# Kernel optimization log

Hardware: AMD Instinct MI355X
Metric: run time of the kernel (lower is better)

Reference implementation:

```python
import jax, jax.numpy as jnp
import numpy as np

N_NODES = 100000
N_EDGES = 3200000
NFEAT, H1, H2, NCLASS = 512, 300, 200, 40


def setup_inputs() -> dict:
    key = jax.random.key(0)
    ks = jax.random.split(key, 8)
    x = jax.random.normal(ks[0], (N_NODES, NFEAT), dtype=jnp.float32)
    edge_index = jax.random.randint(ks[1], (2, N_EDGES), 0, N_NODES, dtype=jnp.int32)
    edge_weight = jax.random.uniform(ks[2], (N_EDGES,), dtype=jnp.float32)
    def glorot(k, fi, fo):
        s = 1.0 / np.sqrt(fi)
        return jax.random.uniform(k, (fi, fo), jnp.float32, -s, s)
    w1 = glorot(ks[3], NFEAT, H1)
    w2 = glorot(ks[4], H1, H2)
    w3 = glorot(ks[5], H2, NCLASS)
    return {
        'x': x, 'edge_index': edge_index, 'edge_weight': edge_weight,
        'w1': w1, 'b1': jnp.zeros((H1,), jnp.float32),
        'w2': w2, 'b2': jnp.zeros((H2,), jnp.float32),
        'w3': w3, 'b3': jnp.zeros((NCLASS,), jnp.float32),
    }


def _gcn_layer(h, edge_index, edge_weight, w, b):
    # support = h @ W ; out = A @ support + b  (A given as weighted edge list)
    support = h @ w                                   # [N, out]
    src, dst = edge_index[0], edge_index[1]
    msgs = support[src] * edge_weight[:, None]        # gather + scale, [E, out]
    agg = jax.ops.segment_sum(msgs, dst, num_segments=h.shape[0])
    return agg + b


def reference(x, edge_index, edge_weight, w1, b1, w2, b2, w3, b3):
    h1 = jax.nn.relu(_gcn_layer(x, edge_index, edge_weight, w1, b1))
    h2 = jax.nn.relu(_gcn_layer(h1, edge_index, edge_weight, w2, b2))
    logits = _gcn_layer(h2, edge_index, edge_weight, w3, b3)
    return jax.nn.softmax(logits, axis=1)
```

## Files before the change

kernel.cpp:

```cpp
#include <hip/hip_runtime.h>
#include <hip/hip_bf16.h>
#include <hip/hip_fp16.h>
#include <math.h>

#define NFEAT 512
#define H1 300
#define H2 200
#define NCLASS 40

typedef __attribute__((ext_vector_type(8))) _Float16 half8;
typedef __attribute__((ext_vector_type(4))) float f32x4;
typedef __attribute__((ext_vector_type(2))) unsigned int u32x2;

__device__ __forceinline__ void stage16(const void* gptr, void* ldsptr) {
    __builtin_amdgcn_global_load_lds(
        (const __attribute__((address_space(1))) unsigned int*)gptr,
        (__attribute__((address_space(3))) unsigned int*)ldsptr,
        16, 0, 0);
}

__device__ __forceinline__ unsigned short f2h(float f) {
    return __half_as_ushort(__float2half(f));
}
__device__ __forceinline__ float h2f(unsigned short u) {
    return __half2float(__ushort_as_half(u));
}
__device__ __forceinline__ float2 h2f2(unsigned int u) {
    __half2 h = *reinterpret_cast<__half2*>(&u);
    return __half22float2(h);
}
__device__ __forceinline__ unsigned pack2h(float a, float b) {
    return (unsigned)f2h(a) | ((unsigned)f2h(b) << 16);
}


__global__ __launch_bounds__(256) void count_dst_kernel(const int* __restrict__ dst,
                                                        int* __restrict__ counts, int E) {
    int i = blockIdx.x * blockDim.x + threadIdx.x;
    if (i < E) atomicAdd(&counts[dst[i]], 1);
}

__global__ __launch_bounds__(1024) void scan_kernel(const int* __restrict__ counts,
                                                    int* __restrict__ row_ptr,
                                                    int* __restrict__ nextp, int N) {
    __shared__ int sums[1024];
    const int tid = threadIdx.x;
    const int CH = (N + 1023) >> 10;
    const int b = tid * CH;
    const int e = min(b + CH, N);
    int s = 0;
    for (int i = b; i < e; i++) s += counts[i];
    sums[tid] = s;
    __syncthreads();
    #pragma unroll
    for (int off = 1; off < 1024; off <<= 1) {
        int t = (tid >= off) ? sums[tid - off] : 0;
        __syncthreads();
        sums[tid] += t;
        __syncthreads();
    }
    int run = (tid > 0) ? sums[tid - 1] : 0;
    for (int i = b; i < e; i++) {
        row_ptr[i] = run;
        nextp[i] = run;
        run += counts[i];
    }
    if (tid == 0) row_ptr[N] = sums[1023];
}

__global__ __launch_bounds__(256) void fill_csr_kernel(const int* __restrict__ src,
                                                       const int* __restrict__ dst,
                                                       const float* __restrict__ ew,
                                                       int* __restrict__ next,
                                                       int2* __restrict__ csr_sw, int E) {
    int i = blockIdx.x * blockDim.x + threadIdx.x;
    if (i < E) {
        int d = dst[i];
        int pos = atomicAdd(&next[d], 1);
        csr_sw[pos] = make_int2(src[i], __float_as_int(ew[i]));
    }
}


__global__ __launch_bounds__(256) void cvt_x_kernel(const float* __restrict__ in,
                                                    unsigned short* __restrict__ out,
                                                    size_t n4) {
    size_t i = (size_t)blockIdx.x * 256 + threadIdx.x;
    if (i < n4) {
        float4 a = ((const float4*)in)[i];
        u32x2 w;
        w.x = pack2h(a.x, a.y);
        w.y = pack2h(a.z, a.w);
        *(u32x2*)(out + i * 4) = w;
    }
}


__global__ __launch_bounds__(256) void split_weights_kernel(
        const float* __restrict__ w1, const float* __restrict__ w2, const float* __restrict__ w3,
        unsigned short* __restrict__ W1H, unsigned short* __restrict__ W1L,
        unsigned short* __restrict__ W2H, unsigned short* __restrict__ W2L,
        unsigned short* __restrict__ W3H, unsigned short* __restrict__ W3L) {
    int i = blockIdx.x * 256 + threadIdx.x;
    const float* w; unsigned short *H, *L; int K, N, KP;
    if (i < 163840) {
        w = w1; H = W1H; L = W1L; K = 512; N = 300; KP = 512;
    } else if (i < 163840 + 81920) {
        i -= 163840; w = w2; H = W2H; L = W2L; K = 300; N = 200; KP = 320;
    } else {
        i -= 245760; w = w3; H = W3H; L = W3L; K = 200; N = 40; KP = 256;
    }
    int n = i / KP, k = i - n * KP;
    float a = (n < N && k < K) ? w[(size_t)k * N + n] : 0.f;
    unsigned short h = f2h(a);
    H[i] = h;
    L[i] = f2h(a - h2f(h));
}


template <int KPAD, int NT>
__global__ __launch_bounds__(256, 3) void gemm_f16_kernel(
        const unsigned short* __restrict__ A,
        const unsigned short* __restrict__ Bhi, const unsigned short* __restrict__ Blo,
        unsigned short* __restrict__ C, int M, int NP, int MT) {
    extern __shared__ short lds[];
    short* As    = lds;
    short* Bs_hi = lds + 16384;
    short* Bs_lo = lds + 20480;

    const int id = blockIdx.x;
    const int g  = id / (8 * NT);
    const int r  = id % (8 * NT);
    const int nt = r >> 3;
    const int x  = r & 7;
    const int mt = g * 8 + x;
    if (mt >= MT) return;

    const int tid = threadIdx.x;
    const int wave = tid >> 6, lane = tid & 63;
    const int lm = lane & 15, quad = lane >> 4;
    const int bm = mt * 256, bn = nt * 64;

    f32x4 acc[4][4] = {};

    for (int k0 = 0; k0 < KPAD; k0 += 64) {
        #pragma unroll
        for (int i = 0; i < 8; i++) {
            int t = i * 256 + tid;
            int m = t >> 3;
            int c = (t & 7) ^ (m & 7);
            int row = bm + m; row = row < M ? row : M - 1;
            size_t goff = (size_t)row * KPAD + (size_t)(k0 + c * 8);
            int lbase = (i * 256 + wave * 64) * 8;
            stage16(A + goff, As + lbase);
        }
        #pragma unroll
        for (int i = 0; i < 2; i++) {
            int t = i * 256 + tid;
            int n = t >> 3;
            int c = (t & 7) ^ (n & 7);
            size_t goff = (size_t)(bn + n) * KPAD + (size_t)(k0 + c * 8);
            int lbase = (i * 256 + wave * 64) * 8;
            stage16(Bhi + goff, Bs_hi + lbase);
            stage16(Blo + goff, Bs_lo + lbase);
        }
        __syncthreads();

        #pragma unroll
        for (int h = 0; h < 2; h++) {
            const int cidx = h * 4 + quad;
            half8 a[4], bh[4], bl[4];
            #pragma unroll
            for (int i = 0; i < 4; i++) {
                int m = wave * 64 + i * 16 + lm;
                int off = (m * 8 + (cidx ^ (m & 7))) * 8;
                a[i] = *(const half8*)(As + off);
            }
            #pragma unroll
            for (int j = 0; j < 4; j++) {
                int n = j * 16 + lm;
                int off = (n * 8 + (cidx ^ (n & 7))) * 8;
                bh[j] = *(const half8*)(Bs_hi + off);
                bl[j] = *(const half8*)(Bs_lo + off);
            }
            #pragma unroll
            for (int i = 0; i < 4; i++)
                #pragma unroll
                for (int j = 0; j < 4; j++) {
                    acc[i][j] = __builtin_amdgcn_mfma_f32_16x16x32_f16(a[i], bh[j], acc[i][j], 0, 0, 0);
                    acc[i][j] = __builtin_amdgcn_mfma_f32_16x16x32_f16(a[i], bl[j], acc[i][j], 0, 0, 0);
                }
        }
        __syncthreads();
    }

    #pragma unroll
    for (int i = 0; i < 4; i++) {
        #pragma unroll
        for (int j = 0; j < 4; j++) {
            #pragma unroll
            for (int r2 = 0; r2 < 4; r2++) {
                int row = bm + wave * 64 + i * 16 + quad * 4 + r2;
                int col = bn + j * 16 + lm;
                if (row < M)
                    C[(size_t)row * NP + col] = f2h(acc[i][j][r2]);
            }
        }
    }
}


template <int F, int NP>
__global__ __launch_bounds__(256) void spmm_relu_f16_kernel(
        const int* __restrict__ row_ptr, const int2* __restrict__ csr_sw,
        const unsigned short* __restrict__ support, const float* __restrict__ bias,
        unsigned short* __restrict__ outp, int N) {
    constexpr int F4 = F / 4;
    constexpr int NP4 = NP / 4;
    constexpr int NCH = (F4 + 63) / 64;
    constexpr int NCHW = (NP4 + 63) / 64;

    int row = blockIdx.x * 4 + (threadIdx.x >> 6);
    int lane = threadIdx.x & 63;
    if (row >= N) return;
    int beg = row_ptr[row], end = row_ptr[row + 1];

    float acc[NCHW][4] = {};

    int e = beg;
    for (; e + 3 < end; e += 4) {
        int s_[4]; float w_[4];
        #pragma unroll
        for (int q = 0; q < 4; q++) {
            int2 sw = csr_sw[e + q];
            s_[q] = __builtin_amdgcn_readfirstlane(sw.x);
            w_[q] = __uint_as_float((unsigned)__builtin_amdgcn_readfirstlane(sw.y));
        }
        u32x2 u[4][NCH];
        #pragma unroll
        for (int q = 0; q < 4; q++) {
            const unsigned short* sp = support + (size_t)s_[q] * NP;
            #pragma unroll
            for (int j = 0; j < NCH; j++) {
                int f4 = j * 64 + lane;
                if (f4 < F4) u[q][j] = *(const u32x2*)(sp + f4 * 4);
            }
        }
        #pragma unroll
        for (int q = 0; q < 4; q++) {
            #pragma unroll
            for (int j = 0; j < NCH; j++) {
                int f4 = j * 64 + lane;
                if (f4 < F4) {
                    float2 a0 = h2f2(u[q][j].x), a1 = h2f2(u[q][j].y);
                    acc[j][0] += w_[q] * a0.x;
                    acc[j][1] += w_[q] * a0.y;
                    acc[j][2] += w_[q] * a1.x;
                    acc[j][3] += w_[q] * a1.y;
                }
            }
        }
    }
    for (; e < end; e++) {
        int2 sw = csr_sw[e];
        int ssrc = __builtin_amdgcn_readfirstlane(sw.x);
        float w0 = __uint_as_float((unsigned)__builtin_amdgcn_readfirstlane(sw.y));
        const unsigned short* sp = support + (size_t)ssrc * NP;
        #pragma unroll
        for (int j = 0; j < NCH; j++) {
            int f4 = j * 64 + lane;
            if (f4 < F4) {
                u32x2 u = *(const u32x2*)(sp + f4 * 4);
                float2 a0 = h2f2(u.x), a1 = h2f2(u.y);
                acc[j][0] += w0 * a0.x;
                acc[j][1] += w0 * a0.y;
                acc[j][2] += w0 * a1.x;
                acc[j][3] += w0 * a1.y;
            }
        }
    }

    #pragma unroll
    for (int j = 0; j < NCHW; j++) {
        int f4 = j * 64 + lane;
        if (f4 < NP4) {
            bool real = f4 < F4;
            float4 bb = real ? ((const float4*)bias)[f4] : make_float4(0, 0, 0, 0);
            float v0 = real ? fmaxf(acc[j][0] + bb.x, 0.f) : 0.f;
            float v1 = real ? fmaxf(acc[j][1] + bb.y, 0.f) : 0.f;
            float v2 = real ? fmaxf(acc[j][2] + bb.z, 0.f) : 0.f;
            float v3 = real ? fmaxf(acc[j][3] + bb.w, 0.f) : 0.f;
            u32x2 w;
            w.x = pack2h(v0, v1);
            w.y = pack2h(v2, v3);
            *(u32x2*)(outp + (size_t)row * NP + f4 * 4) = w;
        }
    }
}

__global__ __launch_bounds__(256) void spmm_softmax_kernel(
        const int* __restrict__ row_ptr, const int2* __restrict__ csr_sw,
        const unsigned short* __restrict__ support, const float* __restrict__ bias,
        float* __restrict__ out, int N) {
    int row = blockIdx.x * 4 + (threadIdx.x >> 6);
    int lane = threadIdx.x & 63;
    if (row >= N) return;
    int beg = row_ptr[row], end = row_ptr[row + 1];
    const bool act = lane < NCLASS / 4;
    float acc[4] = {0.f, 0.f, 0.f, 0.f};
    int e = beg;
    for (; e + 1 < end; e += 2) {
        int2 sw0 = csr_sw[e];
        int2 sw1 = csr_sw[e + 1];
        int  s0 = __builtin_amdgcn_readfirstlane(sw0.x);
        int  s1 = __builtin_amdgcn_readfirstlane(sw1.x);
        float w0 = __uint_as_float((unsigned)__builtin_amdgcn_readfirstlane(sw0.y));
        float w1 = __uint_as_float((unsigned)__builtin_amdgcn_readfirstlane(sw1.y));
        if (act) {
            u32x2 u0 = *(const u32x2*)(support + (size_t)s0 * 64 + lane * 4);
            u32x2 u1 = *(const u32x2*)(support + (size_t)s1 * 64 + lane * 4);
            float2 a0 = h2f2(u0.x), a1 = h2f2(u0.y);
            float2 c0 = h2f2(u1.x), c1 = h2f2(u1.y);
            acc[0] += w0 * a0.x + w1 * c0.x;
            acc[1] += w0 * a0.y + w1 * c0.y;
            acc[2] += w0 * a1.x + w1 * c1.x;
            acc[3] += w0 * a1.y + w1 * c1.y;
        }
    }
    if (e < end) {
        int2 sw = csr_sw[e];
        int  s0 = __builtin_amdgcn_readfirstlane(sw.x);
        float w0 = __uint_as_float((unsigned)__builtin_amdgcn_readfirstlane(sw.y));
        if (act) {
            u32x2 u = *(const u32x2*)(support + (size_t)s0 * 64 + lane * 4);
            float2 a0 = h2f2(u.x), a1 = h2f2(u.y);
            acc[0] += w0 * a0.x;
            acc[1] += w0 * a0.y;
            acc[2] += w0 * a1.x;
            acc[3] += w0 * a1.y;
        }
    }
    float v[4];
    float m = -INFINITY;
    if (act) {
        float4 bb = ((const float4*)bias)[lane];
        v[0] = acc[0] + bb.x; v[1] = acc[1] + bb.y;
        v[2] = acc[2] + bb.z; v[3] = acc[3] + bb.w;
        m = fmaxf(fmaxf(v[0], v[1]), fmaxf(v[2], v[3]));
    }
    #pragma unroll
    for (int off = 8; off; off >>= 1) m = fmaxf(m, __shfl_xor(m, off));
    float s = 0.f, ex[4];
    if (act) {
        #pragma unroll
        for (int k = 0; k < 4; k++) { ex[k] = expf(v[k] - m); s += ex[k]; }
    }
    #pragma unroll
    for (int off = 8; off; off >>= 1) s += __shfl_xor(s, off);
    if (act) {
        float inv = 1.f / s;
        float4 r = make_float4(ex[0] * inv, ex[1] * inv, ex[2] * inv, ex[3] * inv);
        ((float4*)(out + (size_t)row * NCLASS))[lane] = r;
    }
}


extern "C" void kernel_launch(void* const* d_in, const int* in_sizes, int n_in,
                              void* d_out, int out_size, void* d_ws, size_t ws_size,
                              hipStream_t stream) {
    const float* x   = (const float*)d_in[0];
    const int*   ei  = (const int*)d_in[1];
    const float* ew  = (const float*)d_in[2];
    const float* w1  = (const float*)d_in[3];
    const float* b1  = (const float*)d_in[4];
    const float* w2  = (const float*)d_in[5];
    const float* b2  = (const float*)d_in[6];
    const float* w3  = (const float*)d_in[7];
    const float* b3  = (const float*)d_in[8];
    float* out = (float*)d_out;

    const int N = in_sizes[0] / NFEAT;
    const int E = in_sizes[2];
    const int* src = ei;
    const int* dst = ei + E;

    const int KP1 = 512, NP1 = 320, NT1 = 5;
    const int KP2 = 320, NP2 = 256, NT2 = 4;
    const int KP3 = 256, NP3 = 64,  NT3 = 1;

    char* base = (char*)d_ws;
    unsigned short* XH  = (unsigned short*)(base);
    unsigned short* H1H = (unsigned short*)(base);
    unsigned short* H2H = (unsigned short*)(base);

    unsigned short* support = (unsigned short*)(base + 102400256);

    size_t wo = 102400256 + 64000256;
    auto walloc = [&](size_t bytes) { void* r = base + wo; wo += (bytes + 255) & ~(size_t)255; return r; };
    unsigned short* W1H = (unsigned short*)walloc((size_t)NP1 * KP1 * 2);
    unsigned short* W1L = (unsigned short*)walloc((size_t)NP1 * KP1 * 2);
    unsigned short* W2H = (unsigned short*)walloc((size_t)NP2 * KP2 * 2);
    unsigned short* W2L = (unsigned short*)walloc((size_t)NP2 * KP2 * 2);
    unsigned short* W3H = (unsigned short*)walloc((size_t)NP3 * KP3 * 2);
    unsigned short* W3L = (unsigned short*)walloc((size_t)NP3 * KP3 * 2);
    int*  counts  = (int*)walloc((size_t)N * 4);
    int*  row_ptr = (int*)walloc((size_t)(N + 1) * 4);
    int*  nextp   = (int*)walloc((size_t)N * 4);
    int2* csr_sw  = (int2*)walloc((size_t)E * 8);

    const int LDS_BYTES = 48 * 1024;
    const int MT = (N + 255) / 256;
    const int G  = (MT + 7) / 8;
    const int wgs = (N + 3) / 4;

    hipMemsetAsync(counts, 0, (size_t)N * 4, stream);
    count_dst_kernel<<<(E + 255) / 256, 256, 0, stream>>>(dst, counts, E);
    scan_kernel<<<1, 1024, 0, stream>>>(counts, row_ptr, nextp, N);
    fill_csr_kernel<<<(E + 255) / 256, 256, 0, stream>>>(src, dst, ew, nextp, csr_sw, E);

    {
        size_t nx4 = (size_t)N * NFEAT / 4;
        cvt_x_kernel<<<(int)((nx4 + 255) / 256), 256, 0, stream>>>(x, XH, nx4);
    }
    split_weights_kernel<<<1024, 256, 0, stream>>>(w1, w2, w3, W1H, W1L, W2H, W2L, W3H, W3L);

    gemm_f16_kernel<KP1, NT1><<<G * 8 * NT1, 256, LDS_BYTES, stream>>>(
        XH, W1H, W1L, support, N, NP1, MT);
    spmm_relu_f16_kernel<H1, NP1><<<wgs, 256, 0, stream>>>(row_ptr, csr_sw, support, b1, H1H, N);

    gemm_f16_kernel<KP2, NT2><<<G * 8 * NT2, 256, LDS_BYTES, stream>>>(
        H1H, W2H, W2L, support, N, NP2, MT);
    spmm_relu_f16_kernel<H2, NP2><<<wgs, 256, 0, stream>>>(row_ptr, csr_sw, support, b2, H2H, N);

    gemm_f16_kernel<KP3, NT3><<<G * 8 * NT3, 256, LDS_BYTES, stream>>>(
        H2H, W3H, W3L, support, N, NP3, MT);
    spmm_softmax_kernel<<<wgs, 256, 0, stream>>>(row_ptr, csr_sw, support, b3, out, N);
}
```

Before: 1.757 ms.

## Fuse fp32-to-fp16 conversion into first GEMM and load A directly from global

Drops the separate x conversion kernel and has the first GEMM read fp32 x straight from global memory, converting to fp16 in registers. All GEMMs now skip LDS staging for A and load it per-lane from global, keeping only the B tiles in static LDS. The softmax SpMM is also reworked so three groups of 20 lanes each handle a different edge, and the partial sums are combined with shuffles. This trades an extra full pass over x and a kernel launch for uncoalesced, repeated A loads from global across the N tiles, which may hurt GEMM efficiency.

```diff
diff --git a/kernel.cpp b/kernel.cpp
--- a/kernel.cpp
+++ b/kernel.cpp
@@ -82,20 +82,6 @@
 }
 
 
-__global__ __launch_bounds__(256) void cvt_x_kernel(const float* __restrict__ in,
-                                                    unsigned short* __restrict__ out,
-                                                    size_t n4) {
-    size_t i = (size_t)blockIdx.x * 256 + threadIdx.x;
-    if (i < n4) {
-        float4 a = ((const float4*)in)[i];
-        u32x2 w;
-        w.x = pack2h(a.x, a.y);
-        w.y = pack2h(a.z, a.w);
-        *(u32x2*)(out + i * 4) = w;
-    }
-}
-
-
 __global__ __launch_bounds__(256) void split_weights_kernel(
         const float* __restrict__ w1, const float* __restrict__ w2, const float* __restrict__ w3,
         unsigned short* __restrict__ W1H, unsigned short* __restrict__ W1L,
@@ -118,15 +104,13 @@
 }
 
 
-template <int KPAD, int NT>
+template <int KPAD, int NT, bool AF32>
 __global__ __launch_bounds__(256, 3) void gemm_f16_kernel(
-        const unsigned short* __restrict__ A,
+        const void* __restrict__ A_,
         const unsigned short* __restrict__ Bhi, const unsigned short* __restrict__ Blo,
         unsigned short* __restrict__ C, int M, int NP, int MT) {
-    extern __shared__ short lds[];
-    short* As    = lds;
-    short* Bs_hi = lds + 16384;
-    short* Bs_lo = lds + 20480;
+    __shared__ short Bs_hi[4096];
+    __shared__ short Bs_lo[4096];
 
     const int id = blockIdx.x;
     const int g  = id / (8 * NT);
@@ -144,16 +128,6 @@
     f32x4 acc[4][4] = {};
 
     for (int k0 = 0; k0 < KPAD; k0 += 64) {
-        #pragma unroll
-        for (int i = 0; i < 8; i++) {
-            int t = i * 256 + tid;
-            int m = t >> 3;
-            int c = (t & 7) ^ (m & 7);
-            int row = bm + m; row = row < M ? row : M - 1;
-            size_t goff = (size_t)row * KPAD + (size_t)(k0 + c * 8);
-            int lbase = (i * 256 + wave * 64) * 8;
-            stage16(A + goff, As + lbase);
-        }
         #pragma unroll
         for (int i = 0; i < 2; i++) {
             int t = i * 256 + tid;
@@ -172,9 +146,22 @@
             half8 a[4], bh[4], bl[4];
             #pragma unroll
             for (int i = 0; i < 4; i++) {
-                int m = wave * 64 + i * 16 + lm;
-                int off = (m * 8 + (cidx ^ (m & 7))) * 8;
-                a[i] = *(const half8*)(As + off);
+                int row = bm + wave * 64 + i * 16 + lm;
+                row = row < M ? row : M - 1;
+                size_t off = (size_t)row * KPAD + (size_t)(k0 + cidx * 8);
+                if (AF32) {
+                    const float* ap = (const float*)A_ + off;
+                    float4 p = *(const float4*)ap;
+                    float4 q = *(const float4*)(ap + 4);
+                    half8 t8;
+                    t8[0] = (_Float16)p.x; t8[1] = (_Float16)p.y;
+                    t8[2] = (_Float16)p.z; t8[3] = (_Float16)p.w;
+                    t8[4] = (_Float16)q.x; t8[5] = (_Float16)q.y;
+                    t8[6] = (_Float16)q.z; t8[7] = (_Float16)q.w;
+                    a[i] = t8;
+                } else {
+                    a[i] = *(const half8*)((const unsigned short*)A_ + off);
+                }
             }
             #pragma unroll
             for (int j = 0; j < 4; j++) {
@@ -298,6 +285,7 @@
     }
 }
 
+
 __global__ __launch_bounds__(256) void spmm_softmax_kernel(
         const int* __restrict__ row_ptr, const int2* __restrict__ csr_sw,
         const unsigned short* __restrict__ support, const float* __restrict__ bias,
@@ -306,61 +294,43 @@
     int lane = threadIdx.x & 63;
     if (row >= N) return;
     int beg = row_ptr[row], end = row_ptr[row + 1];
-    const bool act = lane < NCLASS / 4;
-    float acc[4] = {0.f, 0.f, 0.f, 0.f};
-    int e = beg;
-    for (; e + 1 < end; e += 2) {
-        int2 sw0 = csr_sw[e];
-        int2 sw1 = csr_sw[e + 1];
-        int  s0 = __builtin_amdgcn_readfirstlane(sw0.x);
-        int  s1 = __builtin_amdgcn_readfirstlane(sw1.x);
-        float w0 = __uint_as_float((unsigned)__builtin_amdgcn_readfirstlane(sw0.y));
-        float w1 = __uint_as_float((unsigned)__builtin_amdgcn_readfirstlane(sw1.y));
-        if (act) {
-            u32x2 u0 = *(const u32x2*)(support + (size_t)s0 * 64 + lane * 4);
-            u32x2 u1 = *(const u32x2*)(support + (size_t)s1 * 64 + lane * 4);
-            float2 a0 = h2f2(u0.x), a1 = h2f2(u0.y);
-            float2 c0 = h2f2(u1.x), c1 = h2f2(u1.y);
-            acc[0] += w0 * a0.x + w1 * c0.x;
-            acc[1] += w0 * a0.y + w1 * c0.y;
-            acc[2] += w0 * a1.x + w1 * c1.x;
-            acc[3] += w0 * a1.y + w1 * c1.y;
-        }
-    }
-    if (e < end) {
-        int2 sw = csr_sw[e];
-        int  s0 = __builtin_amdgcn_readfirstlane(sw.x);
-        float w0 = __uint_as_float((unsigned)__builtin_amdgcn_readfirstlane(sw.y));
-        if (act) {
-            u32x2 u = *(const u32x2*)(support + (size_t)s0 * 64 + lane * 4);
-            float2 a0 = h2f2(u.x), a1 = h2f2(u.y);
-            acc[0] += w0 * a0.x;
-            acc[1] += w0 * a0.y;
-            acc[2] += w0 * a1.x;
-            acc[3] += w0 * a1.y;
-        }
-    }
-    float v[4];
-    float m = -INFINITY;
+
+    const int g = lane / 20;
+    const int t = lane - g * 20;
+    const bool lact = lane < 60;
+
+    float a0 = 0.f, a1 = 0.f;
+    for (int e = beg; e < end; e += 3) {
+        int ei = e + g;
+        bool v = lact && (ei < end);
+        int2 sw = csr_sw[v ? ei : beg];
+        float w = v ? __int_as_float(sw.y) : 0.f;
+        unsigned u = *(const unsigned*)(support + (size_t)sw.x * 64 + t * 2);
+        float2 aa = h2f2(u);
+        a0 += w * aa.x;
+        a1 += w * aa.y;
+    }
+    a0 += __shfl(a0, lane + 20) + __shfl(a0, lane + 40);
+    a1 += __shfl(a1, lane + 20) + __shfl(a1, lane + 40);
+
+    const bool act = lane < 20;
+    float v0 = 0.f, v1 = 0.f, m = -INFINITY;
     if (act) {
-        float4 bb = ((const float4*)bias)[lane];
-        v[0] = acc[0] + bb.x; v[1] = acc[1] + bb.y;
-        v[2] = acc[2] + bb.z; v[3] = acc[3] + bb.w;
-        m = fmaxf(fmaxf(v[0], v[1]), fmaxf(v[2], v[3]));
+        float2 bb = ((const float2*)bias)[t];
+        v0 = a0 + bb.x;
+        v1 = a1 + bb.y;
+        m = fmaxf(v0, v1);
     }
     #pragma unroll
-    for (int off = 8; off; off >>= 1) m = fmaxf(m, __shfl_xor(m, off));
-    float s = 0.f, ex[4];
-    if (act) {
-        #pragma unroll
-        for (int k = 0; k < 4; k++) { ex[k] = expf(v[k] - m); s += ex[k]; }
-    }
+    for (int off = 16; off; off >>= 1) m = fmaxf(m, __shfl_xor(m, off));
+    float e0 = 0.f, e1 = 0.f;
+    if (act) { e0 = expf(v0 - m); e1 = expf(v1 - m); }
+    float s = e0 + e1;
     #pragma unroll
-    for (int off = 8; off; off >>= 1) s += __shfl_xor(s, off);
+    for (int off = 16; off; off >>= 1) s += __shfl_xor(s, off);
     if (act) {
         float inv = 1.f / s;
-        float4 r = make_float4(ex[0] * inv, ex[1] * inv, ex[2] * inv, ex[3] * inv);
-        ((float4*)(out + (size_t)row * NCLASS))[lane] = r;
+        *(float2*)(out + (size_t)row * NCLASS + t * 2) = make_float2(e0 * inv, e1 * inv);
     }
 }
 
@@ -389,7 +359,6 @@
     const int KP3 = 256, NP3 = 64,  NT3 = 1;
 
     char* base = (char*)d_ws;
-    unsigned short* XH  = (unsigned short*)(base);
     unsigned short* H1H = (unsigned short*)(base);
     unsigned short* H2H = (unsigned short*)(base);
 
@@ -408,7 +377,6 @@
     int*  nextp   = (int*)walloc((size_t)N * 4);
     int2* csr_sw  = (int2*)walloc((size_t)E * 8);
 
-    const int LDS_BYTES = 48 * 1024;
     const int MT = (N + 255) / 256;
     const int G  = (MT + 7) / 8;
     const int wgs = (N + 3) / 4;
@@ -418,21 +386,17 @@
     scan_kernel<<<1, 1024, 0, stream>>>(counts, row_ptr, nextp, N);
     fill_csr_kernel<<<(E + 255) / 256, 256, 0, stream>>>(src, dst, ew, nextp, csr_sw, E);
 
-    {
-        size_t nx4 = (size_t)N * NFEAT / 4;
-        cvt_x_kernel<<<(int)((nx4 + 255) / 256), 256, 0, stream>>>(x, XH, nx4);
-    }
     split_weights_kernel<<<1024, 256, 0, stream>>>(w1, w2, w3, W1H, W1L, W2H, W2L, W3H, W3L);
 
-    gemm_f16_kernel<KP1, NT1><<<G * 8 * NT1, 256, LDS_BYTES, stream>>>(
-        XH, W1H, W1L, support, N, NP1, MT);
+    gemm_f16_kernel<KP1, NT1, true><<<G * 8 * NT1, 256, 0, stream>>>(
+        x, W1H, W1L, support, N, NP1, MT);
     spmm_relu_f16_kernel<H1, NP1><<<wgs, 256, 0, stream>>>(row_ptr, csr_sw, support, b1, H1H, N);
 
-    gemm_f16_kernel<KP2, NT2><<<G * 8 * NT2, 256, LDS_BYTES, stream>>>(
+    gemm_f16_kernel<KP2, NT2, false><<<G * 8 * NT2, 256, 0, stream>>>(
         H1H, W2H, W2L, support, N, NP2, MT);
     spmm_relu_f16_kernel<H2, NP2><<<wgs, 256, 0, stream>>>(row_ptr, csr_sw, support, b2, H2H, N);
 
-    gemm_f16_kernel<KP3, NT3><<<G * 8 * NT3, 256, LDS_BYTES, stream>>>(
+    gemm_f16_kernel<KP3, NT3, false><<<G * 8 * NT3, 256, 0, stream>>>(
         H2H, W3H, W3L, support, N, NP3, MT);
     spmm_softmax_kernel<<<wgs, 256, 0, stream>>>(row_ptr, csr_sw, support, b3, out, N);
 }
```

Measured after the change: 1.670 ms. 5.0% less time.
